# Kernel tuning notes

Hardware: AMD Instinct MI355X
Metric: run time of the kernel (lower is better)

The kernel has to match this reference:

```python
import jax, jax.numpy as jnp
import numpy as np

N, DEG = 20000, 16
E = N * DEG
D_IN, D_HID, D_OUT, L = 1024, 512, 128, 3


def setup_inputs() -> dict:
    key = jax.random.key(0)
    ks = jax.random.split(key, 16)
    scale = 0.02
    X = jax.random.normal(ks[0], (N, D_IN), dtype=jnp.float32)
    senders = jax.random.randint(ks[1], (E,), 0, N)
    receivers = jnp.repeat(jnp.arange(N), DEG)  # sorted, every node has DEG neighbors
    inp = {"X": X, "senders": senders, "receivers": receivers}
    ki = 2
    for l in range(L):
        din = D_IN >> l
        dh = D_HID >> l
        inp[f"lw{l}"] = jax.random.normal(ks[ki], (2 * din, dh), jnp.float32) * scale; ki += 1
        inp[f"lb{l}"] = jnp.zeros((dh,), jnp.float32)
        inp[f"aw{l}"] = jax.random.normal(ks[ki], (din, dh), jnp.float32) * scale; ki += 1
        inp[f"aq{l}"] = jax.random.normal(ks[ki], (dh,), jnp.float32) * scale; ki += 1
    inp["ow"] = jax.random.normal(ks[ki], (D_HID >> (L - 1), D_OUT), jnp.float32) * scale
    inp["ob"] = jnp.zeros((D_OUT,), jnp.float32)
    return inp


def _attend(h, senders, receivers, aw, aq):
    # scores depend only on the neighbor (sender) embedding: q @ relu(W h_j)
    logits = jnp.einsum('nh,h->n', jax.nn.relu(h @ aw), aq)            # [N]
    el = logits[senders]                                               # [E]
    m = jax.ops.segment_max(el, receivers, num_segments=N)            # per-receiver max
    w = jnp.exp(el - m[receivers])                                     # [E]
    denom = jax.ops.segment_sum(w, receivers, num_segments=N)         # [N]
    msg = jax.ops.segment_sum(w[:, None] * h[senders], receivers, num_segments=N)  # [N,D]
    return msg / denom[:, None]


def reference(X, senders, receivers,
              lw0, lb0, aw0, aq0,
              lw1, lb1, aw1, aq1,
              lw2, lb2, aw2, aq2,
              ow, ob):
    params = [(lw0, lb0, aw0, aq0), (lw1, lb1, aw1, aq1), (lw2, lb2, aw2, aq2)]
    h = X
    for lw, lb, aw, aq in params:
        hN = _attend(h, senders, receivers, aw, aq)
        h = jax.nn.relu(jnp.concatenate([h, hN], axis=1) @ lw + lb)
    return h[14] @ ow + ob
```

## Files before the change

### kernel.cpp

```cpp
#include <hip/hip_runtime.h>
#include <math.h>

typedef unsigned short ushort_t;
typedef __attribute__((ext_vector_type(8))) short short8;
typedef __attribute__((ext_vector_type(4))) float f32x4;

#define NN    20000
#define DEG   16
constexpr int MAXL2 = 1 + DEG;
constexpr int MAXL1 = MAXL2 + MAXL2*DEG;
constexpr int MAXL0 = MAXL1*DEG;
constexpr int L0PAD = 73 * 64;
constexpr int NWBLK = 512;

__device__ __forceinline__ ushort_t f2bf(float f) {
    unsigned u = __float_as_uint(f);
    return (ushort_t)((u + 0x7FFFu + ((u >> 16) & 1u)) >> 16);
}

__global__ __launch_bounds__(256)
void k_frontier(const int* __restrict__ senders,
                int* list2, int* inv2, int* list1, int* inv1,
                int* list0, int* inv0, int* list3, int* cnts, float4* zp, int n4) {
    int t = threadIdx.x;
    if (blockIdx.x > 0) {
        int i = (blockIdx.x - 1) * 256 + t;
        if (i < n4) zp[i] = make_float4(0.f, 0.f, 0.f, 0.f);
        return;
    }
    __shared__ unsigned bm[625];
    __shared__ int cnt;
    auto clear = [&]() { for (int i = t; i < 625; i += 256) bm[i] = 0u; if (t == 0) cnt = 0; };
    auto tryadd = [&](int node, int* list, int* inv) {
        unsigned bit = 1u << (node & 31);
        unsigned old = atomicOr(&bm[node >> 5], bit);
        if (!(old & bit)) { int p = atomicAdd(&cnt, 1); list[p] = node; inv[node] = p; }
    };
    clear(); __syncthreads();
    if (t < 17) { int node = (t < 16) ? senders[14 * DEG + t] : 14; tryadd(node, list2, inv2); }
    __syncthreads();
    int c2 = cnt; if (t == 0) cnts[2] = c2;
    __syncthreads(); clear(); __syncthreads();
    for (int i = t; i < c2 * 17; i += 256) {
        int r = i / 17, k = i - 17 * r;
        int node = (k < 16) ? senders[list2[r] * DEG + k] : list2[r];
        tryadd(node, list1, inv1);
    }
    __syncthreads();
    int c1 = cnt; if (t == 0) cnts[1] = c1;
    __syncthreads(); clear(); __syncthreads();
    for (int i = t; i < c1 * 16; i += 256) {
        int r = i >> 4, k = i & 15;
        tryadd(senders[list1[r] * DEG + k], list0, inv0);
    }
    __syncthreads();
    if (t == 0) { cnts[0] = cnt; cnts[3] = 1; list3[0] = 14; }
}

__global__ __launch_bounds__(256)
void k_prep(const float* __restrict__ W, ushort_t* __restrict__ WT,
            const float* __restrict__ X, const int* __restrict__ list0,
            const int* __restrict__ cnt0, ushort_t* __restrict__ Xg) {
    int t = threadIdx.x;
    if (blockIdx.x < NWBLK) {
        __shared__ float tile[32][33];
        int b = blockIdx.x;
        int bx = b & 15, by = b >> 4;
        int i0 = t >> 3, j0 = (t & 7) * 4;
        int k = by * 32 + i0, n0 = bx * 32;
        float4 v = *(const float4*)(W + (size_t)k * 512 + n0 + j0);
        tile[i0][j0] = v.x; tile[i0][j0 + 1] = v.y; tile[i0][j0 + 2] = v.z; tile[i0][j0 + 3] = v.w;
        __syncthreads();
        int n = n0 + i0, kc = j0;
        ushort_t* p = WT + (size_t)n * 1024 + by * 32 + kc;
        p[0] = f2bf(tile[kc][i0]); p[1] = f2bf(tile[kc + 1][i0]);
        p[2] = f2bf(tile[kc + 2][i0]); p[3] = f2bf(tile[kc + 3][i0]);
    } else {
        int r = blockIdx.x - NWBLK;
        int rc = *cnt0;
        ushort_t o0 = 0, o1 = 0, o2 = 0, o3 = 0;
        if (r < rc) {
            float4 v = *(const float4*)(X + (size_t)list0[r] * 1024 + t * 4);
            o0 = f2bf(v.x); o1 = f2bf(v.y); o2 = f2bf(v.z); o3 = f2bf(v.w);
        }
        ushort_t* p = Xg + (size_t)r * 1024 + t * 4;
        p[0] = o0; p[1] = o1; p[2] = o2; p[3] = o3;
    }
}

__global__ __launch_bounds__(256)
void k_logits_mfma(const ushort_t* __restrict__ Xg,
                   const ushort_t* __restrict__ WT,
                   const float* __restrict__ aq, float* __restrict__ lgc,
                   const int* __restrict__ cnt, int K) {
    __shared__ short As[64 * 40];
    __shared__ short Bs[64 * 40];
    int rcnt = *cnt;
    int row0 = blockIdx.x * 64;
    if (row0 >= rcnt) return;
    int col0 = blockIdx.y * 64;
    int t = threadIdx.x;
    int w = t >> 6, lane = t & 63;

    int sr = t >> 2, sk = (t & 3) * 8;
    const ushort_t* ap = Xg + (size_t)(row0 + sr) * K + sk;
    const ushort_t* bp = WT + (size_t)(col0 + sr) * K + sk;

    int fm = lane & 15, fq = lane >> 4;
    const short* arow = As + (w * 16 + fm) * 40 + fq * 8;
    const short* brow = Bs + fm * 40 + fq * 8;

    f32x4 acc0 = {0.f,0.f,0.f,0.f}, acc1 = {0.f,0.f,0.f,0.f};
    f32x4 acc2 = {0.f,0.f,0.f,0.f}, acc3 = {0.f,0.f,0.f,0.f};

    short8 pa = *(const short8*)(ap);
    short8 pb = *(const short8*)(bp);
    for (int k0 = 0; k0 < K; k0 += 32) {
        *(short8*)(As + sr * 40 + sk) = pa;
        *(short8*)(Bs + sr * 40 + sk) = pb;
        __syncthreads();
        if (k0 + 32 < K) {
            pa = *(const short8*)(ap + k0 + 32);
            pb = *(const short8*)(bp + k0 + 32);
        }
        short8 af = *(const short8*)arow;
        short8 b0 = *(const short8*)(brow);
        short8 b1 = *(const short8*)(brow + 16 * 40);
        short8 b2 = *(const short8*)(brow + 32 * 40);
        short8 b3 = *(const short8*)(brow + 48 * 40);
        acc0 = __builtin_amdgcn_mfma_f32_16x16x32_bf16(af, b0, acc0, 0, 0, 0);
        acc1 = __builtin_amdgcn_mfma_f32_16x16x32_bf16(af, b1, acc1, 0, 0, 0);
        acc2 = __builtin_amdgcn_mfma_f32_16x16x32_bf16(af, b2, acc2, 0, 0, 0);
        acc3 = __builtin_amdgcn_mfma_f32_16x16x32_bf16(af, b3, acc3, 0, 0, 0);
        __syncthreads();
    }

    float aqv0 = aq[col0 + fm], aqv1 = aq[col0 + 16 + fm];
    float aqv2 = aq[col0 + 32 + fm], aqv3 = aq[col0 + 48 + fm];
#pragma unroll
    for (int r = 0; r < 4; r++) {
        float v = fmaxf(acc0[r], 0.f) * aqv0 + fmaxf(acc1[r], 0.f) * aqv1
                + fmaxf(acc2[r], 0.f) * aqv2 + fmaxf(acc3[r], 0.f) * aqv3;
#pragma unroll
        for (int off = 1; off < 16; off <<= 1) v += __shfl_xor(v, off);
        if (fm == 0) atomicAdd(&lgc[row0 + w * 16 + fq * 4 + r], v);
    }
}

__global__ __launch_bounds__(256)
void k_matmul(const float* __restrict__ A1, const float* __restrict__ A2,
              const int* __restrict__ list, const int* __restrict__ inv,
              const float* __restrict__ B, const float* __restrict__ aq,
              float* __restrict__ C, const int* __restrict__ cnt,
              int amode, int omode, int K1, int K2, int NC, int KS) {
    __shared__ float As[32][68];
    __shared__ float Bs[32][64];
    __shared__ float rowsum[64];

    int rcnt = *cnt;
    int row0 = blockIdx.x * 64;
    if (row0 >= rcnt) return;
    int col0 = blockIdx.y * 64;
    int K = K1 + K2;
    int kbeg = blockIdx.z * KS;
    int kend = kbeg + KS; if (kend > K) kend = K;

    int t = threadIdx.x;
    int ty = t >> 4, tx = t & 15;
    int lr = t >> 2, kaoff = (t & 3) * 4;
    int grow = row0 + lr;
    bool rowValid = grow < rcnt;
    const float* rp1 = A1;
    const float* rp2 = A2;
    if (rowValid) {
        int hrow;
        if (amode == 0) hrow = grow;
        else { int node = list[grow]; hrow = (amode == 2) ? inv[node] : node; }
        rp1 = A1 + (size_t)hrow * K1;
        rp2 = A2 + (size_t)grow * K2;
    }
    const float* Bp = B + col0;
    int bidx0 = t, bidx1 = t + 256;

    auto loadA = [&](int k) -> float4 {
        if (!rowValid) return make_float4(0.f, 0.f, 0.f, 0.f);
        const float* src = (k < K1) ? (rp1 + k) : (rp2 + (k - K1));
        return *(const float4*)src;
    };
    auto loadB = [&](int idx, int k0) -> float4 {
        int row = idx >> 4, c4 = (idx & 15) * 4;
        return *(const float4*)(Bp + (size_t)(k0 + row) * NC + c4);
    };

    float4 pa0 = loadA(kbeg + kaoff);
    float4 pa1 = loadA(kbeg + kaoff + 16);
    float4 pb0 = loadB(bidx0, kbeg);
    float4 pb1 = loadB(bidx1, kbeg);

    float acc[4][4] = {};
    for (int k0 = kbeg; k0 < kend; k0 += 32) {
        As[kaoff + 0][lr] = pa0.x; As[kaoff + 1][lr] = pa0.y;
        As[kaoff + 2][lr] = pa0.z; As[kaoff + 3][lr] = pa0.w;
        As[kaoff + 16][lr] = pa1.x; As[kaoff + 17][lr] = pa1.y;
        As[kaoff + 18][lr] = pa1.z; As[kaoff + 19][lr] = pa1.w;
        *(float4*)&Bs[bidx0 >> 4][(bidx0 & 15) * 4] = pb0;
        *(float4*)&Bs[bidx1 >> 4][(bidx1 & 15) * 4] = pb1;
        __syncthreads();
        if (k0 + 32 < kend) {
            pa0 = loadA(k0 + 32 + kaoff);
            pa1 = loadA(k0 + 32 + kaoff + 16);
            pb0 = loadB(bidx0, k0 + 32);
            pb1 = loadB(bidx1, k0 + 32);
        }
#pragma unroll
        for (int kk = 0; kk < 32; kk++) {
            float4 a4 = *(const float4*)&As[kk][ty * 4];
            float4 b4 = *(const float4*)&Bs[kk][tx * 4];
            float a[4] = {a4.x, a4.y, a4.z, a4.w};
            float b[4] = {b4.x, b4.y, b4.z, b4.w};
#pragma unroll
            for (int i = 0; i < 4; i++)
#pragma unroll
                for (int j = 0; j < 4; j++) acc[i][j] += a[i] * b[j];
        }
        __syncthreads();
    }

    if (omode == 0) {
#pragma unroll
        for (int i = 0; i < 4; i++) {
            int r = row0 + ty * 4 + i;
            if (r < rcnt) {
                float* Crow = C + (size_t)r * NC + col0 + tx * 4;
#pragma unroll
                for (int j = 0; j < 4; j++) atomicAdd(&Crow[j], acc[i][j]);
            }
        }
    } else {
        if (t < 64) rowsum[t] = 0.f;
        __syncthreads();
        float aqv[4];
#pragma unroll
        for (int j = 0; j < 4; j++) aqv[j] = aq[col0 + tx * 4 + j];
#pragma unroll
        for (int i = 0; i < 4; i++) {
            float s = 0.f;
#pragma unroll
            for (int j = 0; j < 4; j++) {
                float v = acc[i][j];
                v = v > 0.f ? v : 0.f;
                s += v * aqv[j];
            }
            atomicAdd(&rowsum[ty * 4 + i], s);
        }
        __syncthreads();
        if (t < 64) {
            int r = row0 + t;
            if (r < rcnt) atomicAdd(&C[r], rowsum[t]);
        }
    }
}

__global__ void k_bias_relu(const float* __restrict__ C, const float* __restrict__ b,
                            float* __restrict__ H, const int* __restrict__ cnt, int ncShift) {
    int rcnt = *cnt;
    int NC = 1 << ncShift;
    int e = blockIdx.x * 256 + threadIdx.x;
    int r = e >> ncShift;
    if (r >= rcnt) return;
    int c = e & (NC - 1);
    float v = C[(size_t)r * NC + c] + b[c];
    H[(size_t)r * NC + c] = v > 0.f ? v : 0.f;
}

__global__ __launch_bounds__(256)
void k_agg(const float* __restrict__ Hsrc, const int* __restrict__ invH,
           const float* __restrict__ lgc, const int* __restrict__ invL,
           const int* __restrict__ senders,
           const int* __restrict__ listN, const int* __restrict__ cntN,
           float* __restrict__ hN, int din) {
    __shared__ int   s_row[DEG];
    __shared__ float s_w[DEG];
    __shared__ float s_scale;
    int b = blockIdx.x;
    if (b >= *cntN) return;
    int n = listN[b];
    int t = threadIdx.x;
    if (t < DEG) {
        int s = senders[n * DEG + t];
        s_row[t] = invH ? invH[s] : s;
        s_w[t] = lgc[invL ? invL[s] : s];
    }
    __syncthreads();
    if (t == 0) {
        float m = -1e30f;
        for (int k = 0; k < DEG; k++) m = fmaxf(m, s_w[k]);
        float d = 0.f;
        for (int k = 0; k < DEG; k++) { float w = expf(s_w[k] - m); s_w[k] = w; d += w; }
        s_scale = 1.f / d;
    }
    __syncthreads();
    float scale = s_scale;
    for (int dI = t; dI < din; dI += 256) {
        float acc = 0.f;
#pragma unroll
        for (int k = 0; k < DEG; k++)
            acc += s_w[k] * Hsrc[(size_t)s_row[k] * din + dI];
        hN[(size_t)b * din + dI] = acc * scale;
    }
}

__global__ __launch_bounds__(512)
void k_out(const float* __restrict__ C2, const float* __restrict__ lb2,
           const float* __restrict__ OW, const float* __restrict__ OB,
           float* __restrict__ out) {
    __shared__ float h3s[128];
    __shared__ float part[4][128];
    int t = threadIdx.x;
    if (t < 128) { float v = C2[t] + lb2[t]; h3s[t] = v > 0.f ? v : 0.f; }
    __syncthreads();
    int j = t & 127, s = t >> 7;
    float a = 0.f;
    for (int k = s * 32; k < s * 32 + 32; k++) a += h3s[k] * OW[(size_t)k * 128 + j];
    part[s][j] = a;
    __syncthreads();
    if (t < 128) out[t] = OB[t] + part[0][t] + part[1][t] + part[2][t] + part[3][t];
}

extern "C" void kernel_launch(void* const* d_in, const int* in_sizes, int n_in,
                              void* d_out, int out_size, void* d_ws, size_t ws_size,
                              hipStream_t stream) {
    const float* X       = (const float*)d_in[0];
    const int*   senders = (const int*)d_in[1];
    const float* lw0 = (const float*)d_in[3];
    const float* lb0 = (const float*)d_in[4];
    const float* aw0 = (const float*)d_in[5];
    const float* aq0 = (const float*)d_in[6];
    const float* lw1 = (const float*)d_in[7];
    const float* lb1 = (const float*)d_in[8];
    const float* aw1 = (const float*)d_in[9];
    const float* aq1 = (const float*)d_in[10];
    const float* lw2 = (const float*)d_in[11];
    const float* lb2 = (const float*)d_in[12];
    const float* aw2 = (const float*)d_in[13];
    const float* aq2 = (const float*)d_in[14];
    const float* owp = (const float*)d_in[15];
    const float* obp = (const float*)d_in[16];
    float* out = (float*)d_out;

    char* ws = (char*)d_ws;
    size_t off = 0;
    auto alloc = [&](size_t nbytes) -> void* {
        void* p = ws + off;
        off += (nbytes + 255) & ~(size_t)255;
        return p;
    };
    float* lgc0 = (float*)alloc(L0PAD * 4);
    float* lgc1 = (float*)alloc(MAXL1 * 4);
    float* lgc2 = (float*)alloc(MAXL2 * 4);
    float* C0   = (float*)alloc((size_t)MAXL1 * 512 * 4);
    float* C1   = (float*)alloc((size_t)MAXL2 * 256 * 4);
    float* C2   = (float*)alloc(128 * 4);
    size_t zero_end = off;
    int* inv0  = (int*)alloc(NN * 4);
    int* inv1  = (int*)alloc(NN * 4);
    int* inv2  = (int*)alloc(NN * 4);
    int* list0 = (int*)alloc(L0PAD * 4);
    int* list1 = (int*)alloc(MAXL1 * 4);
    int* list2 = (int*)alloc(MAXL2 * 4);
    int* list3 = (int*)alloc(4);
    int* cnts  = (int*)alloc(4 * 4);
    ushort_t* Xg  = (ushort_t*)alloc((size_t)L0PAD * 1024 * 2);
    ushort_t* awT = (ushort_t*)alloc((size_t)512 * 1024 * 2);
    float* hN0c = (float*)alloc((size_t)MAXL1 * 1024 * 4);
    float* h1c  = (float*)alloc((size_t)MAXL1 * 512 * 4);
    float* hN1c = (float*)alloc((size_t)MAXL2 * 512 * 4);
    float* h2c  = (float*)alloc((size_t)MAXL2 * 256 * 4);
    float* hN2c = (float*)alloc(256 * 4);
    (void)in_sizes; (void)n_in; (void)out_size; (void)ws_size;

    int nz4 = (int)(zero_end / 16);
    int nzb = (nz4 + 255) / 256;

    hipLaunchKernelGGL(k_frontier, dim3(1 + nzb), dim3(256), 0, stream,
                       senders, list2, inv2, list1, inv1, list0, inv0, list3, cnts,
                       (float4*)ws, nz4);
    hipLaunchKernelGGL(k_prep, dim3(NWBLK + L0PAD), dim3(256), 0, stream,
                       aw0, awT, X, list0, cnts + 0, Xg);

    hipLaunchKernelGGL(k_logits_mfma, dim3(73, 512 / 64, 1), dim3(256), 0, stream,
                       Xg, awT, aq0, lgc0, cnts + 0, 1024);
    hipLaunchKernelGGL(k_agg, dim3(MAXL1), dim3(256), 0, stream,
                       X, (const int*)nullptr, lgc0, inv0, senders, list1, cnts + 1, hN0c, 1024);
    hipLaunchKernelGGL(k_matmul, dim3((MAXL1 + 63) / 64, 512 / 64, 8), dim3(256), 0, stream,
                       X, hN0c, list1, (int*)nullptr, lw0, aq0, C0, cnts + 1,
                       1, 0, 1024, 1024, 512, 256);
    hipLaunchKernelGGL(k_bias_relu, dim3((MAXL1 * 512 + 255) / 256), dim3(256), 0, stream,
                       C0, lb0, h1c, cnts + 1, 9);

    hipLaunchKernelGGL(k_matmul, dim3((MAXL1 + 63) / 64, 256 / 64, 1), dim3(256), 0, stream,
                       h1c, h1c, list1, (int*)nullptr, aw1, aq1, lgc1, cnts + 1,
                       0, 1, 512, 0, 256, 512);
    hipLaunchKernelGGL(k_agg, dim3(MAXL2), dim3(256), 0, stream,
                       h1c, inv1, lgc1, inv1, senders, list2, cnts + 2, hN1c, 512);
    hipLaunchKernelGGL(k_matmul, dim3(1, 256 / 64, 8), dim3(256), 0, stream,
                       h1c, hN1c, list2, inv1, lw1, aq1, C1, cnts + 2,
                       2, 0, 512, 512, 256, 128);
    hipLaunchKernelGGL(k_bias_relu, dim3((MAXL2 * 256 + 255) / 256), dim3(256), 0, stream,
                       C1, lb1, h2c, cnts + 2, 8);

    hipLaunchKernelGGL(k_matmul, dim3(1, 128 / 64, 1), dim3(256), 0, stream,
                       h2c, h2c, list2, (int*)nullptr, aw2, aq2, lgc2, cnts + 2,
                       0, 1, 256, 0, 128, 256);
    hipLaunchKernelGGL(k_agg, dim3(1), dim3(256), 0, stream,
                       h2c, inv2, lgc2, inv2, senders, list3, cnts + 3, hN2c, 256);
    hipLaunchKernelGGL(k_matmul, dim3(1, 128 / 64, 4), dim3(256), 0, stream,
                       h2c, hN2c, list3, inv2, lw2, aq2, C2, cnts + 3,
                       2, 0, 256, 256, 128, 128);
    hipLaunchKernelGGL(k_out, dim3(1), dim3(512), 0, stream, C2, lb2, owp, obp, out);
}
```

Baseline: 281.1 us.

## Drop layer-0 dedup, fuse weight transposes, and collapse layers 1-2 into tail kernels

The frontier kernel no longer deduplicates the layer-0 node set. It uses list1 times 16 sender slots directly, and it now also transposes aw0 and aw1 to bf16. Layer-1 logits run on the MFMA kernel with a bf16 copy of h1 written by bias_relu. Aggregation plus the lw1 matmul are fused into k_tail1, and all of layer 2 plus the output projection into a single-block k_tail2. This removes many small launches and the serial dedup pass, and k_agg is vectorized with float4. The cost is duplicated layer-0 rows and a reduction-order change from using a bf16 h1 for the logits.

```diff
diff --git a/kernel.cpp b/kernel.cpp
--- a/kernel.cpp
+++ b/kernel.cpp
@@ -9,83 +9,96 @@
 #define DEG   16
 constexpr int MAXL2 = 1 + DEG;
 constexpr int MAXL1 = MAXL2 + MAXL2*DEG;
-constexpr int MAXL0 = MAXL1*DEG;
 constexpr int L0PAD = 73 * 64;
-constexpr int NWBLK = 512;
 
 __device__ __forceinline__ ushort_t f2bf(float f) {
     unsigned u = __float_as_uint(f);
     return (ushort_t)((u + 0x7FFFu + ((u >> 16) & 1u)) >> 16);
 }
 
+__device__ void transpose_tile(const float* __restrict__ W, ushort_t* __restrict__ WT,
+                               int b, int nshift, int K) {
+    __shared__ float tile[32][33];
+    int t = threadIdx.x;
+    int N = 32 << nshift;
+    int bx = b & ((1 << nshift) - 1), by = b >> nshift;
+    int i0 = t >> 3, j0 = (t & 7) * 4;
+    int k = by * 32 + i0, n0 = bx * 32;
+    float4 v = *(const float4*)(W + (size_t)k * N + n0 + j0);
+    tile[i0][j0] = v.x; tile[i0][j0 + 1] = v.y; tile[i0][j0 + 2] = v.z; tile[i0][j0 + 3] = v.w;
+    __syncthreads();
+    int n = n0 + i0, kc = j0;
+    ushort_t* p = WT + (size_t)n * K + by * 32 + kc;
+    p[0] = f2bf(tile[kc][i0]);     p[1] = f2bf(tile[kc + 1][i0]);
+    p[2] = f2bf(tile[kc + 2][i0]); p[3] = f2bf(tile[kc + 3][i0]);
+}
+
 __global__ __launch_bounds__(256)
 void k_frontier(const int* __restrict__ senders,
-                int* list2, int* inv2, int* list1, int* inv1,
-                int* list0, int* inv0, int* list3, int* cnts, float4* zp, int n4) {
-    int t = threadIdx.x;
-    if (blockIdx.x > 0) {
-        int i = (blockIdx.x - 1) * 256 + t;
-        if (i < n4) zp[i] = make_float4(0.f, 0.f, 0.f, 0.f);
+                int* __restrict__ list2, int* __restrict__ inv2,
+                int* __restrict__ list1, int* __restrict__ inv1,
+                int* __restrict__ cnts,
+                const float* __restrict__ aw0, ushort_t* __restrict__ awT,
+                const float* __restrict__ aw1, ushort_t* __restrict__ awT1,
+                float4* __restrict__ zp, int n4, int nzb) {
+    int t = threadIdx.x;
+    int bb = (int)blockIdx.x;
+    if (bb > 0) {
+        int b = bb - 1;
+        if (b < nzb) {
+            int i = b * 256 + t;
+            if (i < n4) zp[i] = make_float4(0.f, 0.f, 0.f, 0.f);
+            return;
+        }
+        b -= nzb;
+        if (b < 512) { transpose_tile(aw0, awT, b, 4, 1024); return; }
+        b -= 512;
+        transpose_tile(aw1, awT1, b, 3, 512);
         return;
     }
     __shared__ unsigned bm[625];
     __shared__ int cnt;
+    __shared__ int lloc[MAXL2];
     auto clear = [&]() { for (int i = t; i < 625; i += 256) bm[i] = 0u; if (t == 0) cnt = 0; };
-    auto tryadd = [&](int node, int* list, int* inv) {
+    clear(); __syncthreads();
+    if (t < 17) {
+        int node = (t < 16) ? senders[14 * DEG + t] : 14;
         unsigned bit = 1u << (node & 31);
         unsigned old = atomicOr(&bm[node >> 5], bit);
-        if (!(old & bit)) { int p = atomicAdd(&cnt, 1); list[p] = node; inv[node] = p; }
-    };
-    clear(); __syncthreads();
-    if (t < 17) { int node = (t < 16) ? senders[14 * DEG + t] : 14; tryadd(node, list2, inv2); }
-    __syncthreads();
-    int c2 = cnt; if (t == 0) cnts[2] = c2;
+        if (!(old & bit)) { int p = atomicAdd(&cnt, 1); list2[p] = node; inv2[node] = p; lloc[p] = node; }
+    }
+    __syncthreads();
+    int c2 = cnt;
+    if (t == 0) cnts[2] = c2;
     __syncthreads(); clear(); __syncthreads();
     for (int i = t; i < c2 * 17; i += 256) {
-        int r = i / 17, k = i - 17 * r;
-        int node = (k < 16) ? senders[list2[r] * DEG + k] : list2[r];
-        tryadd(node, list1, inv1);
-    }
-    __syncthreads();
-    int c1 = cnt; if (t == 0) cnts[1] = c1;
-    __syncthreads(); clear(); __syncthreads();
-    for (int i = t; i < c1 * 16; i += 256) {
-        int r = i >> 4, k = i & 15;
-        tryadd(senders[list1[r] * DEG + k], list0, inv0);
-    }
-    __syncthreads();
-    if (t == 0) { cnts[0] = cnt; cnts[3] = 1; list3[0] = 14; }
+        int r = i / 17, k = i - r * 17;
+        int node = (k < 16) ? senders[lloc[r] * DEG + k] : lloc[r];
+        unsigned bit = 1u << (node & 31);
+        unsigned old = atomicOr(&bm[node >> 5], bit);
+        if (!(old & bit)) { int p = atomicAdd(&cnt, 1); list1[p] = node; inv1[node] = p; }
+    }
+    __syncthreads();
+    if (t == 0) { int c1 = cnt; cnts[1] = c1; cnts[0] = c1 * 16; }
 }
 
 __global__ __launch_bounds__(256)
-void k_prep(const float* __restrict__ W, ushort_t* __restrict__ WT,
-            const float* __restrict__ X, const int* __restrict__ list0,
-            const int* __restrict__ cnt0, ushort_t* __restrict__ Xg) {
-    int t = threadIdx.x;
-    if (blockIdx.x < NWBLK) {
-        __shared__ float tile[32][33];
-        int b = blockIdx.x;
-        int bx = b & 15, by = b >> 4;
-        int i0 = t >> 3, j0 = (t & 7) * 4;
-        int k = by * 32 + i0, n0 = bx * 32;
-        float4 v = *(const float4*)(W + (size_t)k * 512 + n0 + j0);
-        tile[i0][j0] = v.x; tile[i0][j0 + 1] = v.y; tile[i0][j0 + 2] = v.z; tile[i0][j0 + 3] = v.w;
-        __syncthreads();
-        int n = n0 + i0, kc = j0;
-        ushort_t* p = WT + (size_t)n * 1024 + by * 32 + kc;
-        p[0] = f2bf(tile[kc][i0]); p[1] = f2bf(tile[kc + 1][i0]);
-        p[2] = f2bf(tile[kc + 2][i0]); p[3] = f2bf(tile[kc + 3][i0]);
-    } else {
-        int r = blockIdx.x - NWBLK;
-        int rc = *cnt0;
-        ushort_t o0 = 0, o1 = 0, o2 = 0, o3 = 0;
-        if (r < rc) {
-            float4 v = *(const float4*)(X + (size_t)list0[r] * 1024 + t * 4);
-            o0 = f2bf(v.x); o1 = f2bf(v.y); o2 = f2bf(v.z); o3 = f2bf(v.w);
-        }
-        ushort_t* p = Xg + (size_t)r * 1024 + t * 4;
-        p[0] = o0; p[1] = o1; p[2] = o2; p[3] = o3;
-    }
+void k_prep(const float* __restrict__ X, const int* __restrict__ senders,
+            const int* __restrict__ list1, const int* __restrict__ cnts,
+            int* __restrict__ inv0, ushort_t* __restrict__ Xg) {
+    int r = blockIdx.x;
+    int t = threadIdx.x;
+    int rc = cnts[0];
+    ushort_t o0 = 0, o1 = 0, o2 = 0, o3 = 0;
+    if (r < rc) {
+        int n = list1[r >> 4];
+        int s = senders[n * DEG + (r & 15)];
+        if (t == 0) inv0[s] = r;
+        float4 v = *(const float4*)(X + (size_t)s * 1024 + t * 4);
+        o0 = f2bf(v.x); o1 = f2bf(v.y); o2 = f2bf(v.z); o3 = f2bf(v.w);
+    }
+    ushort_t* p = Xg + (size_t)r * 1024 + t * 4;
+    p[0] = o0; p[1] = o1; p[2] = o2; p[3] = o3;
 }
 
 __global__ __launch_bounds__(256)
@@ -262,7 +275,8 @@
 }
 
 __global__ void k_bias_relu(const float* __restrict__ C, const float* __restrict__ b,
-                            float* __restrict__ H, const int* __restrict__ cnt, int ncShift) {
+                            float* __restrict__ H, ushort_t* __restrict__ Hb,
+                            const int* __restrict__ cnt, int ncShift) {
     int rcnt = *cnt;
     int NC = 1 << ncShift;
     int e = blockIdx.x * 256 + threadIdx.x;
@@ -270,7 +284,9 @@
     if (r >= rcnt) return;
     int c = e & (NC - 1);
     float v = C[(size_t)r * NC + c] + b[c];
-    H[(size_t)r * NC + c] = v > 0.f ? v : 0.f;
+    v = v > 0.f ? v : 0.f;
+    H[(size_t)r * NC + c] = v;
+    Hb[(size_t)r * NC + c] = f2bf(v);
 }
 
 __global__ __launch_bounds__(256)
@@ -296,35 +312,168 @@
         float m = -1e30f;
         for (int k = 0; k < DEG; k++) m = fmaxf(m, s_w[k]);
         float d = 0.f;
-        for (int k = 0; k < DEG; k++) { float w = expf(s_w[k] - m); s_w[k] = w; d += w; }
+        for (int k = 0; k < DEG; k++) { float w = __expf(s_w[k] - m); s_w[k] = w; d += w; }
         s_scale = 1.f / d;
     }
     __syncthreads();
     float scale = s_scale;
-    for (int dI = t; dI < din; dI += 256) {
+    for (int dI = t * 4; dI < din; dI += 1024) {
+        float4 acc = make_float4(0.f, 0.f, 0.f, 0.f);
+#pragma unroll
+        for (int k = 0; k < DEG; k++) {
+            float w = s_w[k];
+            float4 v = *(const float4*)(Hsrc + (size_t)s_row[k] * din + dI);
+            acc.x += w * v.x; acc.y += w * v.y; acc.z += w * v.z; acc.w += w * v.w;
+        }
+        acc.x *= scale; acc.y *= scale; acc.z *= scale; acc.w *= scale;
+        *(float4*)(hN + (size_t)b * din + dI) = acc;
+    }
+}
+
+__global__ __launch_bounds__(256)
+void k_tail1(const float* __restrict__ h1, const float* __restrict__ lgc1,
+             const int* __restrict__ senders, const int* __restrict__ list2,
+             const int* __restrict__ inv1, const int* __restrict__ cnts,
+             const float* __restrict__ lw1, const float* __restrict__ lb1,
+             float* __restrict__ h2) {
+    __shared__ float As[17][1024];
+    __shared__ float sw[17][16];
+    __shared__ int   srow[17][16];
+    __shared__ int   orow[17];
+    __shared__ float psum[8][17 * 32];
+    int c2 = cnts[2];
+    int t = threadIdx.x;
+    int b = blockIdx.x;
+
+    for (int i = t; i < c2 * 16; i += 256) {
+        int j = i >> 4, k = i & 15;
+        int s = senders[list2[j] * DEG + k];
+        int rr = inv1[s];
+        srow[j][k] = rr;
+        sw[j][k] = lgc1[rr];
+    }
+    if (t < c2) orow[t] = inv1[list2[t]];
+    __syncthreads();
+    if (t < c2) {
+        float m = -1e30f;
+        for (int k = 0; k < 16; k++) m = fmaxf(m, sw[t][k]);
+        float d = 0.f;
+        for (int k = 0; k < 16; k++) { float w = __expf(sw[t][k] - m); sw[t][k] = w; d += w; }
+        float inv = 1.f / d;
+        for (int k = 0; k < 16; k++) sw[t][k] *= inv;
+    }
+    __syncthreads();
+    for (int e = t; e < c2 * 512; e += 256) {
+        int j = e >> 9, d = e & 511;
+        As[j][d] = h1[(size_t)orow[j] * 512 + d];
+        float a = 0.f;
+#pragma unroll
+        for (int k = 0; k < 16; k++) a += sw[j][k] * h1[(size_t)srow[j][k] * 512 + d];
+        As[j][512 + d] = a;
+    }
+    __syncthreads();
+    int c = t & 31, s = t >> 5;
+    int gc = b * 32 + c;
+    float acc[17];
+#pragma unroll
+    for (int j = 0; j < 17; j++) acc[j] = 0.f;
+    for (int k = s * 128; k < s * 128 + 128; k += 4) {
+        float b0 = lw1[(size_t)(k + 0) * 256 + gc];
+        float b1 = lw1[(size_t)(k + 1) * 256 + gc];
+        float b2 = lw1[(size_t)(k + 2) * 256 + gc];
+        float b3 = lw1[(size_t)(k + 3) * 256 + gc];
+#pragma unroll
+        for (int j = 0; j < 17; j++) {
+            float4 a = *(const float4*)&As[j][k];
+            acc[j] += a.x * b0 + a.y * b1 + a.z * b2 + a.w * b3;
+        }
+    }
+#pragma unroll
+    for (int j = 0; j < 17; j++) psum[s][j * 32 + c] = acc[j];
+    __syncthreads();
+    for (int e = t; e < c2 * 32; e += 256) {
+        int j = e >> 5, cc = e & 31;
+        float v = 0.f;
+#pragma unroll
+        for (int s2 = 0; s2 < 8; s2++) v += psum[s2][j * 32 + cc];
+        v += lb1[b * 32 + cc];
+        h2[(size_t)j * 256 + b * 32 + cc] = v > 0.f ? v : 0.f;
+    }
+}
+
+__global__ __launch_bounds__(512)
+void k_tail2(const float* __restrict__ h2, const int* __restrict__ senders,
+             const int* __restrict__ inv2, const int* __restrict__ cnts,
+             const float* __restrict__ aw2, const float* __restrict__ aq2,
+             const float* __restrict__ lw2, const float* __restrict__ lb2,
+             const float* __restrict__ ow, const float* __restrict__ ob,
+             float* __restrict__ out) {
+    __shared__ float sh2[17][256];
+    __shared__ float slog[17];
+    __shared__ float swt[16];
+    __shared__ int   srow2[16];
+    __shared__ float hN2[256];
+    __shared__ float sh3[128];
+    __shared__ float part[4][128];
+    __shared__ int   srow14;
+    int c2 = cnts[2];
+    int t = threadIdx.x;
+    for (int e = t; e < c2 * 256; e += 512) sh2[e >> 8][e & 255] = h2[e];
+    if (t < c2) slog[t] = 0.f;
+    if (t < 16) srow2[t] = inv2[senders[14 * DEG + t]];
+    if (t == 31) srow14 = inv2[14];
+    __syncthreads();
+    for (int p = t; p < c2 * 128; p += 512) {
+        int j = p >> 7, c = p & 127;
+        float dot = 0.f;
+        for (int k = 0; k < 256; k += 4) {
+            float4 a = *(const float4*)&sh2[j][k];
+            dot += a.x * aw2[(k + 0) * 128 + c] + a.y * aw2[(k + 1) * 128 + c]
+                 + a.z * aw2[(k + 2) * 128 + c] + a.w * aw2[(k + 3) * 128 + c];
+        }
+        float v = dot > 0.f ? dot : 0.f;
+        atomicAdd(&slog[j], v * aq2[c]);
+    }
+    __syncthreads();
+    if (t == 0) {
+        float m = -1e30f;
+        for (int k = 0; k < 16; k++) m = fmaxf(m, slog[srow2[k]]);
+        float d = 0.f;
+        for (int k = 0; k < 16; k++) { float w = __expf(slog[srow2[k]] - m); swt[k] = w; d += w; }
+        float inv = 1.f / d;
+        for (int k = 0; k < 16; k++) swt[k] *= inv;
+    }
+    __syncthreads();
+    if (t < 256) {
+        float a = 0.f;
+#pragma unroll
+        for (int k = 0; k < 16; k++) a += swt[k] * sh2[srow2[k]][t];
+        hN2[t] = a;
+    }
+    __syncthreads();
+    {
+        int c = t & 127, s4 = t >> 7;
         float acc = 0.f;
-#pragma unroll
-        for (int k = 0; k < DEG; k++)
-            acc += s_w[k] * Hsrc[(size_t)s_row[k] * din + dI];
-        hN[(size_t)b * din + dI] = acc * scale;
-    }
-}
-
-__global__ __launch_bounds__(512)
-void k_out(const float* __restrict__ C2, const float* __restrict__ lb2,
-           const float* __restrict__ OW, const float* __restrict__ OB,
-           float* __restrict__ out) {
-    __shared__ float h3s[128];
-    __shared__ float part[4][128];
-    int t = threadIdx.x;
-    if (t < 128) { float v = C2[t] + lb2[t]; h3s[t] = v > 0.f ? v : 0.f; }
-    __syncthreads();
-    int j = t & 127, s = t >> 7;
-    float a = 0.f;
-    for (int k = s * 32; k < s * 32 + 32; k++) a += h3s[k] * OW[(size_t)k * 128 + j];
-    part[s][j] = a;
-    __syncthreads();
-    if (t < 128) out[t] = OB[t] + part[0][t] + part[1][t] + part[2][t] + part[3][t];
+        for (int k = s4 * 128; k < s4 * 128 + 128; k++) {
+            float a = (k < 256) ? sh2[srow14][k] : hN2[k - 256];
+            acc += a * lw2[(size_t)k * 128 + c];
+        }
+        part[s4][c] = acc;
+    }
+    __syncthreads();
+    if (t < 128) {
+        float v = part[0][t] + part[1][t] + part[2][t] + part[3][t] + lb2[t];
+        sh3[t] = v > 0.f ? v : 0.f;
+    }
+    __syncthreads();
+    {
+        int o = t & 127, s4 = t >> 7;
+        float acc = 0.f;
+        for (int k = s4 * 32; k < s4 * 32 + 32; k++) acc += sh3[k] * ow[(size_t)k * 128 + o];
+        part[s4][o] = acc;
+    }
+    __syncthreads();
+    if (t < 128) out[t] = ob[t] + part[0][t] + part[1][t] + part[2][t] + part[3][t];
 }
 
 extern "C" void kernel_launch(void* const* d_in, const int* in_sizes, int n_in,
@@ -355,40 +504,34 @@
         off += (nbytes + 255) & ~(size_t)255;
         return p;
     };
-    float* lgc0 = (float*)alloc(L0PAD * 4);
-    float* lgc1 = (float*)alloc(MAXL1 * 4);
-    float* lgc2 = (float*)alloc(MAXL2 * 4);
-    float* C0   = (float*)alloc((size_t)MAXL1 * 512 * 4);
-    float* C1   = (float*)alloc((size_t)MAXL2 * 256 * 4);
-    float* C2   = (float*)alloc(128 * 4);
+    float* lgc0     = (float*)alloc(L0PAD * 4);
+    float* lgc1     = (float*)alloc(320 * 4);
+    float* C0       = (float*)alloc((size_t)MAXL1 * 512 * 4);
+    ushort_t* h1b   = (ushort_t*)alloc((size_t)320 * 512 * 2);
     size_t zero_end = off;
     int* inv0  = (int*)alloc(NN * 4);
     int* inv1  = (int*)alloc(NN * 4);
     int* inv2  = (int*)alloc(NN * 4);
-    int* list0 = (int*)alloc(L0PAD * 4);
     int* list1 = (int*)alloc(MAXL1 * 4);
     int* list2 = (int*)alloc(MAXL2 * 4);
-    int* list3 = (int*)alloc(4);
     int* cnts  = (int*)alloc(4 * 4);
-    ushort_t* Xg  = (ushort_t*)alloc((size_t)L0PAD * 1024 * 2);
-    ushort_t* awT = (ushort_t*)alloc((size_t)512 * 1024 * 2);
+    ushort_t* Xg   = (ushort_t*)alloc((size_t)L0PAD * 1024 * 2);
+    ushort_t* awT  = (ushort_t*)alloc((size_t)512 * 1024 * 2);
+    ushort_t* awT1 = (ushort_t*)alloc((size_t)256 * 512 * 2);
     float* hN0c = (float*)alloc((size_t)MAXL1 * 1024 * 4);
     float* h1c  = (float*)alloc((size_t)MAXL1 * 512 * 4);
-    float* hN1c = (float*)alloc((size_t)MAXL2 * 512 * 4);
     float* h2c  = (float*)alloc((size_t)MAXL2 * 256 * 4);
-    float* hN2c = (float*)alloc(256 * 4);
     (void)in_sizes; (void)n_in; (void)out_size; (void)ws_size;
 
     int nz4 = (int)(zero_end / 16);
     int nzb = (nz4 + 255) / 256;
 
-    hipLaunchKernelGGL(k_frontier, dim3(1 + nzb), dim3(256), 0, stream,
-                       senders, list2, inv2, list1, inv1, list0, inv0, list3, cnts,
-                       (float4*)ws, nz4);
-    hipLaunchKernelGGL(k_prep, dim3(NWBLK + L0PAD), dim3(256), 0, stream,
-                       aw0, awT, X, list0, cnts + 0, Xg);
-
-    hipLaunchKernelGGL(k_logits_mfma, dim3(73, 512 / 64, 1), dim3(256), 0, stream,
+    hipLaunchKernelGGL(k_frontier, dim3(1 + nzb + 512 + 128), dim3(256), 0, stream,
+                       senders, list2, inv2, list1, inv1, cnts,
+                       aw0, awT, aw1, awT1, (float4*)ws, nz4, nzb);
+    hipLaunchKernelGGL(k_prep, dim3(L0PAD), dim3(256), 0, stream,
+                       X, senders, list1, cnts, inv0, Xg);
+    hipLaunchKernelGGL(k_logits_mfma, dim3(73, 8), dim3(256), 0, stream,
                        Xg, awT, aq0, lgc0, cnts + 0, 1024);
     hipLaunchKernelGGL(k_agg, dim3(MAXL1), dim3(256), 0, stream,
                        X, (const int*)nullptr, lgc0, inv0, senders, list1, cnts + 1, hN0c, 1024);
@@ -396,26 +539,11 @@
                        X, hN0c, list1, (int*)nullptr, lw0, aq0, C0, cnts + 1,
                        1, 0, 1024, 1024, 512, 256);
     hipLaunchKernelGGL(k_bias_relu, dim3((MAXL1 * 512 + 255) / 256), dim3(256), 0, stream,
-                       C0, lb0, h1c, cnts + 1, 9);
-
-    hipLaunchKernelGGL(k_matmul, dim3((MAXL1 + 63) / 64, 256 / 64, 1), dim3(256), 0, stream,
-                       h1c, h1c, list1, (int*)nullptr, aw1, aq1, lgc1, cnts + 1,
-                       0, 1, 512, 0, 256, 512);
-    hipLaunchKernelGGL(k_agg, dim3(MAXL2), dim3(256), 0, stream,
-                       h1c, inv1, lgc1, inv1, senders, list2, cnts + 2, hN1c, 512);
-    hipLaunchKernelGGL(k_matmul, dim3(1, 256 / 64, 8), dim3(256), 0, stream,
-                       h1c, hN1c, list2, inv1, lw1, aq1, C1, cnts + 2,
-                       2, 0, 512, 512, 256, 128);
-    hipLaunchKernelGGL(k_bias_relu, dim3((MAXL2 * 256 + 255) / 256), dim3(256), 0, stream,
-                       C1, lb1, h2c, cnts + 2, 8);
-
-    hipLaunchKernelGGL(k_matmul, dim3(1, 128 / 64, 1), dim3(256), 0, stream,
-                       h2c, h2c, list2, (int*)nullptr, aw2, aq2, lgc2, cnts + 2,
-                       0, 1, 256, 0, 128, 256);
-    hipLaunchKernelGGL(k_agg, dim3(1), dim3(256), 0, stream,
-                       h2c, inv2, lgc2, inv2, senders, list3, cnts + 3, hN2c, 256);
-    hipLaunchKernelGGL(k_matmul, dim3(1, 128 / 64, 4), dim3(256), 0, stream,
-                       h2c, hN2c, list3, inv2, lw2, aq2, C2, cnts + 3,
-                       2, 0, 256, 256, 128, 128);
-    hipLaunchKernelGGL(k_out, dim3(1), dim3(512), 0, stream, C2, lb2, owp, obp, out);
-}
+                       C0, lb0, h1c, h1b, cnts + 1, 9);
+    hipLaunchKernelGGL(k_logits_mfma, dim3(5, 4), dim3(256), 0, stream,
+                       h1b, awT1, aq1, lgc1, cnts + 1, 512);
+    hipLaunchKernelGGL(k_tail1, dim3(8), dim3(256), 0, stream,
+                       h1c, lgc1, senders, list2, inv1, cnts, lw1, lb1, h2c);
+    hipLaunchKernelGGL(k_tail2, dim3(1), dim3(512), 0, stream,
+                       h2c, senders, inv2, cnts, aw2, aq2, lw2, lb2, owp, obp, out);
+}
```

New measurement: 328.3 us. 1.17x slower.
